# Kernel optimization log

Hardware: AMD Instinct MI355X
Metric: run time of the kernel (lower is better)

The kernel has to match this reference:

```python
import jax, jax.numpy as jnp
import numpy as np

NUM_TRIPLES = 16_000_000  # N: training triples in the buffer
NUM_NEG = 65_536          # B: proposed negative triples
NUM_IDS = 100_000         # shared id range for heads/relations/tails


def setup_inputs() -> dict:
    key = jax.random.key(0)
    k_neg, k_mt = jax.random.split(key)
    negative_batch = jax.random.randint(k_neg, (NUM_NEG, 3), 0, NUM_IDS, dtype=jnp.int32)
    mapped_triples = jax.random.randint(k_mt, (NUM_TRIPLES, 3), 0, NUM_IDS, dtype=jnp.int32)
    return {"negative_batch": negative_batch, "mapped_triples": mapped_triples}


def _in_sorted(values, sorted_ref):
    """membership test: values[i] in sorted_ref (sorted 1-D array)."""
    idx = jnp.clip(jnp.searchsorted(sorted_ref, values), 0, sorted_ref.shape[0] - 1)
    return sorted_ref[idx] == values


def reference(negative_batch, mapped_triples):
    # Torch original: head_filter[n] = any_b(mt[n,0] == neg[b,0]); same for relation
    # on the head-filtered subset; final_filter[b] = any surviving triple with
    # mt[n,2] == neg[b,2]. Boolean-indexing of mapped_triples is replaced by a
    # mask (identical math, static shapes); O(B*N) broadcast compares replaced by
    # sort + searchsorted membership (same result, far less traffic).
    neg_heads_sorted = jnp.sort(negative_batch[:, 0])
    neg_rels_sorted = jnp.sort(negative_batch[:, 1])
    # [N] bool: triple's head matches ANY negative head AND relation matches ANY negative relation
    surviving = _in_sorted(mapped_triples[:, 0], neg_heads_sorted) & _in_sorted(
        mapped_triples[:, 1], neg_rels_sorted
    )
    # tails of surviving triples; -1 sentinel never matches (ids are >= 0).
    # Empty-survivor case (the torch RuntimeError branch) falls out naturally.
    tails = jnp.where(surviving, mapped_triples[:, 2], jnp.int32(-1))
    tails_sorted = jnp.sort(tails)
    final_filter = _in_sorted(negative_batch[:, 2], tails_sorted)  # [B] bool
    keep_mask = ~final_filter
    # torch returns negative_batch[keep_mask] (data-dependent shape); under jit we
    # return the same rows with filtered rows set to -1, plus the keep mask.
    filtered_negative_batch = jnp.where(keep_mask[:, None], negative_batch, jnp.int32(-1))
    return filtered_negative_batch, keep_mask
```

## Files before the change

kernel.cpp:

```cpp
#include <hip/hip_runtime.h>
#include <stdint.h>

#define NWORDS 3125
#define NWP    3136
#define NVEC   (NWP / 4)
#define SCAN_BLOCKS 1024
#define SCAN_THREADS 512
#define NCHUNK 32
#define CHUNK  (SCAN_BLOCKS / NCHUNK)

typedef int4 __attribute__((aligned(4))) int4_a4;

__global__ void build_hr_kernel(const int* __restrict__ neg, int B,
                                uint32_t* __restrict__ headb,
                                uint32_t* __restrict__ relb) {
    int b = blockIdx.x * blockDim.x + threadIdx.x;
    if (b >= B) return;
    int h = neg[b * 3 + 0];
    int r = neg[b * 3 + 1];
    atomicOr(&headb[h >> 5], 1u << (h & 31));
    atomicOr(&relb[r >> 5], 1u << (r & 31));
}

__global__ __launch_bounds__(SCAN_THREADS, 8) void scan_triples_kernel(
        const int* __restrict__ mt, int N,
        const uint32_t* __restrict__ headb,
        const uint32_t* __restrict__ relb,
        uint32_t* __restrict__ copies) {
    __shared__ __align__(16) uint32_t sh[NWP];
    __shared__ __align__(16) uint32_t sr[NWP];
    __shared__ __align__(16) uint32_t st[NWP];

    uint4* sh4 = (uint4*)sh;
    uint4* sr4 = (uint4*)sr;
    uint4* st4 = (uint4*)st;
    const uint4* hb4 = (const uint4*)headb;
    const uint4* rb4 = (const uint4*)relb;
    for (int i = threadIdx.x; i < NVEC; i += blockDim.x) {
        sh4[i] = hb4[i];
        sr4[i] = rb4[i];
        st4[i] = make_uint4(0u, 0u, 0u, 0u);
    }
    __syncthreads();

    const uint32_t tid = blockIdx.x * blockDim.x + threadIdx.x;
    const uint32_t stride = gridDim.x * blockDim.x;
    const char* __restrict__ base = (const char*)mt;

    for (uint32_t i = tid; i < (uint32_t)(N - 1); i += stride) {
        int4 v = *(const int4_a4*)(base + i * 12u);
        int h = v.x, r = v.y, t = v.z;
        uint32_t hbit = (sh[h >> 5] >> (h & 31)) & 1u;
        uint32_t rbit = (sr[r >> 5] >> (r & 31)) & 1u;
        if (hbit & rbit) {
            uint32_t bit = 1u << (t & 31);
            if (!(st[t >> 5] & bit)) atomicOr(&st[t >> 5], bit);
        }
    }
    if (tid == 0) {
        int h = mt[(size_t)(N - 1) * 3 + 0];
        int r = mt[(size_t)(N - 1) * 3 + 1];
        int t = mt[(size_t)(N - 1) * 3 + 2];
        if (((sh[h >> 5] >> (h & 31)) & 1u) && ((sr[r >> 5] >> (r & 31)) & 1u))
            atomicOr(&st[t >> 5], 1u << (t & 31));
    }

    __syncthreads();
    uint4* dst4 = (uint4*)(copies + (size_t)blockIdx.x * NWP);
    for (int i = threadIdx.x; i < NVEC; i += blockDim.x) dst4[i] = st4[i];
}

__global__ void reduceA_kernel(const uint32_t* __restrict__ copies,
                               uint32_t* __restrict__ partials) {
    int idx = blockIdx.x * blockDim.x + threadIdx.x;
    if (idx >= NCHUNK * NVEC) return;
    int i  = idx % NVEC;
    int ch = idx / NVEC;
    const uint4* c4 = (const uint4*)copies;
    uint4 acc = make_uint4(0u, 0u, 0u, 0u);
    int c0 = ch * CHUNK;
    for (int c = 0; c < CHUNK; ++c) {
        uint4 v = c4[(size_t)(c0 + c) * NVEC + i];
        acc.x |= v.x; acc.y |= v.y; acc.z |= v.z; acc.w |= v.w;
    }
    ((uint4*)partials)[(size_t)ch * NVEC + i] = acc;
}

__global__ void reduceB_kernel(const uint32_t* __restrict__ partials,
                               uint32_t* __restrict__ final_b) {
    int w = blockIdx.x * blockDim.x + threadIdx.x;
    if (w >= NWP) return;
    uint32_t acc = 0u;
#pragma unroll
    for (int c = 0; c < NCHUNK; ++c) acc |= partials[c * NWP + w];
    final_b[w] = acc;
}

__global__ void finalize_kernel(const int* __restrict__ neg, int B,
                                const uint32_t* __restrict__ final_b,
                                int* __restrict__ out) {
    int b = blockIdx.x * blockDim.x + threadIdx.x;
    if (b >= B) return;
    int h = neg[b * 3 + 0];
    int r = neg[b * 3 + 1];
    int t = neg[b * 3 + 2];
    bool filtered = (final_b[t >> 5] >> (t & 31)) & 1u;
    int keep = filtered ? 0 : 1;
    out[b * 3 + 0] = keep ? h : -1;
    out[b * 3 + 1] = keep ? r : -1;
    out[b * 3 + 2] = keep ? t : -1;
    out[3 * B + b] = keep;
}

extern "C" void kernel_launch(void* const* d_in, const int* in_sizes, int n_in,
                              void* d_out, int out_size, void* d_ws, size_t ws_size,
                              hipStream_t stream) {
    const int* neg = (const int*)d_in[0];
    const int* mt  = (const int*)d_in[1];
    int B = in_sizes[0] / 3;
    int N = in_sizes[1] / 3;
    int* out = (int*)d_out;

    uint32_t* ws       = (uint32_t*)d_ws;
    uint32_t* headb    = ws;
    uint32_t* relb     = ws + NWP;
    uint32_t* final_b  = ws + 2 * NWP;
    uint32_t* partials = ws + 3 * NWP;
    uint32_t* copies   = ws + (3 + NCHUNK) * NWP;

    hipMemsetAsync(ws, 0, 2 * NWP * sizeof(uint32_t), stream);
    build_hr_kernel<<<(B + 255) / 256, 256, 0, stream>>>(neg, B, headb, relb);
    scan_triples_kernel<<<SCAN_BLOCKS, SCAN_THREADS, 0, stream>>>(
        mt, N, headb, relb, copies);
    {
        int total = NCHUNK * NVEC;
        reduceA_kernel<<<(total + 255) / 256, 256, 0, stream>>>(copies, partials);
    }
    reduceB_kernel<<<(NWP + 255) / 256, 256, 0, stream>>>(partials, final_b);
    finalize_kernel<<<(B + 255) / 256, 256, 0, stream>>>(neg, B, final_b, out);
}
```

Measured before the change: 57.20 us.

## Merge per-block tail bitmaps via global atomics into striped partials, drop reduce kernels

Instead of writing 1024 full per-block bitmap copies and reducing them in two extra kernels, each scan block atomically ORs its nonzero shared-memory words into one of 8 striped global partial bitmaps. The finalize kernel ORs the 8 partials for each lookup. The memset is replaced by a small zero kernel that also clears the partials. This removes two kernel launches and about 12 MB of copy write and readback, at the cost of global atomic contention at the end of the scan.

```diff
diff --git a/kernel.cpp b/kernel.cpp
--- a/kernel.cpp
+++ b/kernel.cpp
@@ -6,10 +6,14 @@
 #define NVEC   (NWP / 4)
 #define SCAN_BLOCKS 1024
 #define SCAN_THREADS 512
-#define NCHUNK 32
-#define CHUNK  (SCAN_BLOCKS / NCHUNK)
+#define NPART  8
 
 typedef int4 __attribute__((aligned(4))) int4_a4;
+
+__global__ void zero_kernel(uint32_t* __restrict__ w, int n) {
+    int i = blockIdx.x * blockDim.x + threadIdx.x;
+    if (i < n) w[i] = 0u;
+}
 
 __global__ void build_hr_kernel(const int* __restrict__ neg, int B,
                                 uint32_t* __restrict__ headb,
@@ -26,7 +30,7 @@
         const int* __restrict__ mt, int N,
         const uint32_t* __restrict__ headb,
         const uint32_t* __restrict__ relb,
-        uint32_t* __restrict__ copies) {
+        uint32_t* __restrict__ parts) {
     __shared__ __align__(16) uint32_t sh[NWP];
     __shared__ __align__(16) uint32_t sr[NWP];
     __shared__ __align__(16) uint32_t st[NWP];
@@ -66,45 +70,26 @@
     }
 
     __syncthreads();
-    uint4* dst4 = (uint4*)(copies + (size_t)blockIdx.x * NWP);
-    for (int i = threadIdx.x; i < NVEC; i += blockDim.x) dst4[i] = st4[i];
-}
-
-__global__ void reduceA_kernel(const uint32_t* __restrict__ copies,
-                               uint32_t* __restrict__ partials) {
-    int idx = blockIdx.x * blockDim.x + threadIdx.x;
-    if (idx >= NCHUNK * NVEC) return;
-    int i  = idx % NVEC;
-    int ch = idx / NVEC;
-    const uint4* c4 = (const uint4*)copies;
-    uint4 acc = make_uint4(0u, 0u, 0u, 0u);
-    int c0 = ch * CHUNK;
-    for (int c = 0; c < CHUNK; ++c) {
-        uint4 v = c4[(size_t)(c0 + c) * NVEC + i];
-        acc.x |= v.x; acc.y |= v.y; acc.z |= v.z; acc.w |= v.w;
+    uint32_t* dst = parts + (size_t)(blockIdx.x & (NPART - 1)) * NWP;
+    for (int i = threadIdx.x; i < NWORDS; i += blockDim.x) {
+        uint32_t v = st[i];
+        if (v) atomicOr(&dst[i], v);
     }
-    ((uint4*)partials)[(size_t)ch * NVEC + i] = acc;
-}
-
-__global__ void reduceB_kernel(const uint32_t* __restrict__ partials,
-                               uint32_t* __restrict__ final_b) {
-    int w = blockIdx.x * blockDim.x + threadIdx.x;
-    if (w >= NWP) return;
-    uint32_t acc = 0u;
-#pragma unroll
-    for (int c = 0; c < NCHUNK; ++c) acc |= partials[c * NWP + w];
-    final_b[w] = acc;
 }
 
 __global__ void finalize_kernel(const int* __restrict__ neg, int B,
-                                const uint32_t* __restrict__ final_b,
+                                const uint32_t* __restrict__ parts,
                                 int* __restrict__ out) {
     int b = blockIdx.x * blockDim.x + threadIdx.x;
     if (b >= B) return;
     int h = neg[b * 3 + 0];
     int r = neg[b * 3 + 1];
     int t = neg[b * 3 + 2];
-    bool filtered = (final_b[t >> 5] >> (t & 31)) & 1u;
+    int w = t >> 5;
+    uint32_t acc = 0u;
+#pragma unroll
+    for (int c = 0; c < NPART; ++c) acc |= parts[c * NWP + w];
+    bool filtered = (acc >> (t & 31)) & 1u;
     int keep = filtered ? 0 : 1;
     out[b * 3 + 0] = keep ? h : -1;
     out[b * 3 + 1] = keep ? r : -1;
@@ -121,21 +106,15 @@
     int N = in_sizes[1] / 3;
     int* out = (int*)d_out;
 
-    uint32_t* ws       = (uint32_t*)d_ws;
-    uint32_t* headb    = ws;
-    uint32_t* relb     = ws + NWP;
-    uint32_t* final_b  = ws + 2 * NWP;
-    uint32_t* partials = ws + 3 * NWP;
-    uint32_t* copies   = ws + (3 + NCHUNK) * NWP;
+    uint32_t* ws    = (uint32_t*)d_ws;
+    uint32_t* headb = ws;
+    uint32_t* relb  = ws + NWP;
+    uint32_t* parts = ws + 2 * NWP;
 
-    hipMemsetAsync(ws, 0, 2 * NWP * sizeof(uint32_t), stream);
+    zero_kernel<<<((2 + NPART) * NWP + 255) / 256, 256, 0, stream>>>(
+        ws, (2 + NPART) * NWP);
     build_hr_kernel<<<(B + 255) / 256, 256, 0, stream>>>(neg, B, headb, relb);
     scan_triples_kernel<<<SCAN_BLOCKS, SCAN_THREADS, 0, stream>>>(
-        mt, N, headb, relb, copies);
-    {
-        int total = NCHUNK * NVEC;
-        reduceA_kernel<<<(total + 255) / 256, 256, 0, stream>>>(copies, partials);
-    }
-    reduceB_kernel<<<(NWP + 255) / 256, 256, 0, stream>>>(partials, final_b);
-    finalize_kernel<<<(B + 255) / 256, 256, 0, stream>>>(neg, B, final_b, out);
+        mt, N, headb, relb, parts);
+    finalize_kernel<<<(B + 255) / 256, 256, 0, stream>>>(neg, B, parts, out);
 }
```

Measured after the change: 55.83 us. -2.4%, faster.
